# Kernel optimization log

Hardware: AMD Instinct MI355X
Metric: run time of the kernel (lower is better)

## Reference

```python
import jax, jax.numpy as jnp
import numpy as np

B, T, C, H = 4, 2048, 512, 8
D = C // H  # head dim = 64

def setup_inputs() -> dict:
    key = jax.random.key(0)
    ks = jax.random.split(key, 6)
    x = jax.random.normal(ks[0], (B, T, C), dtype=jnp.float32)
    # per-batch graph adjacency mask: True = attend, False = masked
    adj_matrix = jax.random.bernoulli(ks[1], 0.5, (B, T, T))
    # ensure self-edges so no row is fully masked
    adj_matrix = adj_matrix | jnp.eye(T, dtype=bool)[None]
    s = 0.02
    w_qkv = jax.random.normal(ks[2], (C, 3 * C), dtype=jnp.float32) * s
    b_qkv = jnp.zeros((3 * C,), dtype=jnp.float32)
    w_proj = jax.random.normal(ks[3], (C, C), dtype=jnp.float32) * s
    b_proj = jnp.zeros((C,), dtype=jnp.float32)
    return {"x": x, "adj_matrix": adj_matrix, "w_qkv": w_qkv, "b_qkv": b_qkv,
            "w_proj": w_proj, "b_proj": b_proj}

def reference(x, adj_matrix, w_qkv, b_qkv, w_proj, b_proj):
    Bx, Tx, Cx = x.shape
    qkv = x @ w_qkv + b_qkv                       # [B,T,3C]
    q, k, v = jnp.split(qkv, 3, axis=-1)
    def heads(t):
        return t.reshape(Bx, Tx, H, D).transpose(0, 2, 1, 3)  # [B,H,T,D]
    q, k, v = heads(q), heads(k), heads(v)
    scale = 1.0 / jnp.sqrt(jnp.asarray(D, dtype=x.dtype))
    scores = jnp.einsum('bhtd,bhsd->bhts', q, k) * scale      # [B,H,T,T]
    neg = jnp.finfo(scores.dtype).min
    scores = jnp.where(adj_matrix[:, None, :, :], scores, neg)
    attn = jax.nn.softmax(scores, axis=-1)
    y = jnp.einsum('bhts,bhsd->bhtd', attn, v)                # [B,H,T,D]
    y = y.transpose(0, 2, 1, 3).reshape(Bx, Tx, Cx)           # [B,T,C]
    return y @ w_proj + b_proj
```

## Files before the change

### kernel.cpp

```cpp
#include <hip/hip_runtime.h>
#include <stdint.h>

typedef __attribute__((ext_vector_type(8))) __bf16 bf16x8;
typedef __attribute__((ext_vector_type(4))) __bf16 bf16x4;
typedef __attribute__((ext_vector_type(2))) __bf16 bf16x2;
typedef __attribute__((ext_vector_type(4))) float f32x4;
typedef __attribute__((ext_vector_type(16))) float f32x16;
typedef __attribute__((ext_vector_type(4))) unsigned u32x4;
typedef __attribute__((ext_vector_type(2))) int i32x2;

__device__ __forceinline__ unsigned short f2bf(float f) {
  unsigned u = __float_as_uint(f);
  u += 0x7FFFu + ((u >> 16) & 1u);
  return (unsigned short)(u >> 16);
}

__device__ __forceinline__ float exp2fast(float x) {
#if __has_builtin(__builtin_amdgcn_exp2f)
  return __builtin_amdgcn_exp2f(x);
#else
  return __expf(x * 0.6931471805599453f);
#endif
}

__device__ __forceinline__ void pl32swap(unsigned &a, unsigned &b) {
#if __has_builtin(__builtin_amdgcn_permlane32_swap)
  i32x2 r = __builtin_amdgcn_permlane32_swap((int)a, (int)b, false, false);
  a = (unsigned)r[0]; b = (unsigned)r[1];
#else
  asm volatile("v_permlane32_swap_b32 %0, %1" : "+v"(a), "+v"(b));
#endif
}

__device__ __forceinline__ int swz8(int r) { return (r & 7) ^ ((r >> 3) & 3); }

__device__ __forceinline__ void gload16(const unsigned short* src, unsigned short* ldsdst) {
  __builtin_amdgcn_global_load_lds(
      (const __attribute__((address_space(1))) unsigned int*)src,
      (__attribute__((address_space(3))) unsigned int*)ldsdst, 16, 0, 0);
}

__device__ __forceinline__ void stage8(const unsigned short* gbase, long long strideElems,
                                       unsigned short* ldsTile, int rowBase) {
  const int lane = threadIdx.x & 63;
  const int r = rowBase + (lane >> 3);
  const int oct = (lane & 7) ^ swz8(r);
  gload16(gbase + (long long)r * strideElems + oct * 8, ldsTile + rowBase * 64);
}


__global__ __launch_bounds__(256) void prep(const float* __restrict__ x,
                                            unsigned short* __restrict__ xb,
                                            const float* __restrict__ wq,
                                            unsigned short* __restrict__ wqt,
                                            const float* __restrict__ wp,
                                            unsigned short* __restrict__ wpt,
                                            const int* __restrict__ adj,
                                            unsigned long long* __restrict__ mb) {
  int blk = blockIdx.x;
  if (blk < 16384) {
    int tid = blk * 256 + threadIdx.x;
    int4 v = ((const int4*)adj)[tid];
    unsigned n = (v.x != 0 ? 1u : 0u) | (v.y != 0 ? 2u : 0u) |
                 (v.z != 0 ? 4u : 0u) | (v.w != 0 ? 8u : 0u);
    unsigned long long part = (unsigned long long)n << ((threadIdx.x & 15) * 4);
    part |= __shfl_xor(part, 1);
    part |= __shfl_xor(part, 2);
    part |= __shfl_xor(part, 4);
    part |= __shfl_xor(part, 8);
    if ((threadIdx.x & 15) == 0) mb[tid >> 4] = part;
    return;
  }
  blk -= 16384;
  if (blk < 4096) {
    int i = (blk * 256 + threadIdx.x) * 4;
    float4 v = *(const float4*)(x + i);
    ushort4 o;
    o.x = f2bf(v.x); o.y = f2bf(v.y); o.z = f2bf(v.z); o.w = f2bf(v.w);
    *(ushort4*)(xb + i) = o;
    return;
  }
  blk -= 4096;
  const float* w; unsigned short* wt; int N; int bx, by;
  if (blk < 768) { w = wq; wt = wqt; N = 1536; bx = blk & 15; by = blk >> 4; }
  else { blk -= 768; w = wp; wt = wpt; N = 512; bx = blk & 15; by = blk >> 4; }
  __shared__ float tile[32][33];
  int k0 = bx * 32, n0 = by * 32;
  int tx = threadIdx.x & 31, ty = threadIdx.x >> 5;
#pragma unroll
  for (int i = 0; i < 4; i++)
    tile[ty + i * 8][tx] = w[(long long)(k0 + ty + i * 8) * N + n0 + tx];
  __syncthreads();
#pragma unroll
  for (int i = 0; i < 4; i++)
    wt[(long long)(n0 + ty + i * 8) * 512 + k0 + tx] = f2bf(tile[tx][ty + i * 8]);
}


__device__ __forceinline__ void gemm_core(const unsigned short* __restrict__ A,
                                          const unsigned short* __restrict__ Wt,
                                          unsigned short* Al, unsigned short* Bl,
                                          int m0, int n0, f32x4 acc[4][4]) {
  const int lane = threadIdx.x & 63;
  const int wid = threadIdx.x >> 6;
  const int c = lane & 15, g = lane >> 4;
  const int wm = wid >> 1, wn = wid & 1;
  const unsigned short* Ab = A + (long long)m0 * 512;
  const unsigned short* Bb = Wt + (long long)n0 * 512;

  for (int k0 = 0; k0 < 512; k0 += 64) {
    __syncthreads();
#pragma unroll
    for (int i = 0; i < 4; i++) stage8(Ab + k0, 512, Al, wid * 32 + i * 8);
#pragma unroll
    for (int i = 0; i < 4; i++) stage8(Bb + k0, 512, Bl, wid * 32 + i * 8);
    asm volatile("s_waitcnt vmcnt(0)" ::: "memory");
    __syncthreads();
#pragma unroll
    for (int kk = 0; kk < 2; kk++) {
      bf16x8 af[4], bfr[4];
#pragma unroll
      for (int mi = 0; mi < 4; mi++) {
        int row = wm * 64 + mi * 16 + c;
        af[mi] = *(const bf16x8*)&Al[row * 64 + (((kk << 2) | g) ^ swz8(row)) * 8];
      }
#pragma unroll
      for (int ni = 0; ni < 4; ni++) {
        int row = wn * 64 + ni * 16 + c;
        bfr[ni] = *(const bf16x8*)&Bl[row * 64 + (((kk << 2) | g) ^ swz8(row)) * 8];
      }
#pragma unroll
      for (int mi = 0; mi < 4; mi++)
#pragma unroll
        for (int ni = 0; ni < 4; ni++)
          acc[mi][ni] = __builtin_amdgcn_mfma_f32_16x16x32_bf16(af[mi], bfr[ni], acc[mi][ni], 0, 0, 0);
    }
  }
}

__global__ __launch_bounds__(256) void gemm_qkv(const unsigned short* __restrict__ xb,
                                                const unsigned short* __restrict__ wqt,
                                                const float* __restrict__ bqkv,
                                                unsigned short* __restrict__ qb,
                                                unsigned short* __restrict__ kb,
                                                unsigned short* __restrict__ vtb) {
  __shared__ __align__(16) unsigned short Al[128 * 64];
  __shared__ __align__(16) unsigned short Bl[128 * 64];
  f32x4 acc[4][4] = {};
  int m0 = blockIdx.x * 128, n0 = blockIdx.y * 128;
  gemm_core(xb, wqt, Al, Bl, m0, n0, acc);
  const int lane = threadIdx.x & 63;
  const int wid = threadIdx.x >> 6;
  const int c = lane & 15, g = lane >> 4;
  const int wm = wid >> 1, wn = wid & 1;
#pragma unroll
  for (int ni = 0; ni < 4; ni++) {
    int n = n0 + wn * 64 + ni * 16 + c;
    float bv = bqkv[n];
    int which = n >> 9;
    int h = (n & 511) >> 6, d = n & 63;
#pragma unroll
    for (int mi = 0; mi < 4; mi++) {
      int mbase = m0 + wm * 64 + mi * 16 + g * 4;
      int b = mbase >> 11, t0 = mbase & 2047;
      int bh = b * 8 + h;
      if (which == 2) {
        ushort4 o;
        o.x = f2bf(acc[mi][ni][0] + bv); o.y = f2bf(acc[mi][ni][1] + bv);
        o.z = f2bf(acc[mi][ni][2] + bv); o.w = f2bf(acc[mi][ni][3] + bv);
        *(ushort4*)&vtb[((long long)bh * 64 + d) * 2048 + t0] = o;
      } else if (which == 0) {
#pragma unroll
        for (int j = 0; j < 4; j++)
          qb[(bh * 2048 + t0 + j) * 64 + d] = f2bf((acc[mi][ni][j] + bv) * 0.18033688011112042f);
      } else {
#pragma unroll
        for (int j = 0; j < 4; j++)
          kb[(bh * 2048 + t0 + j) * 64 + d] = f2bf(acc[mi][ni][j] + bv);
      }
    }
  }
}

__global__ __launch_bounds__(256) void gemm_proj(const unsigned short* __restrict__ yb,
                                                 const unsigned short* __restrict__ wpt,
                                                 const float* __restrict__ bproj,
                                                 float* __restrict__ out) {
  __shared__ __align__(16) unsigned short Al[128 * 64];
  __shared__ __align__(16) unsigned short Bl[128 * 64];
  f32x4 acc[4][4] = {};
  int m0 = blockIdx.x * 128, n0 = blockIdx.y * 128;
  gemm_core(yb, wpt, Al, Bl, m0, n0, acc);
  const int lane = threadIdx.x & 63;
  const int wid = threadIdx.x >> 6;
  const int c = lane & 15, g = lane >> 4;
  const int wm = wid >> 1, wn = wid & 1;
#pragma unroll
  for (int ni = 0; ni < 4; ni++) {
    int n = n0 + wn * 64 + ni * 16 + c;
    float bv = bproj[n];
#pragma unroll
    for (int mi = 0; mi < 4; mi++) {
      int mbase = m0 + wm * 64 + mi * 16 + g * 4;
#pragma unroll
      for (int j = 0; j < 4; j++)
        out[(long long)(mbase + j) * 512 + n] = acc[mi][ni][j] + bv;
    }
  }
}

__global__ __launch_bounds__(256) void attn(const unsigned short* __restrict__ qb,
                                            const unsigned short* __restrict__ kb,
                                            const unsigned short* __restrict__ vtb,
                                            const unsigned long long* __restrict__ mbits,
                                            unsigned short* __restrict__ yb) {
  __shared__ __align__(16) unsigned short Kl[3][64 * 64];
  __shared__ __align__(16) unsigned short Vl[3][64 * 64];
  __shared__ __align__(16) float lut4[16][4];
  const int lane = threadIdx.x & 63;
  const int w = threadIdx.x >> 6;
  const int l31 = lane & 31, h5 = lane >> 5;
  const int sA = swz8(l31);
  const int bid = blockIdx.x;
  const int bh = bid & 31;
  const int q0 = (bid >> 5) * 128;
  const int b = bh >> 3, h = bh & 7;
  const int qglob = q0 + w * 32 + l31;

  if (threadIdx.x < 16) {
    int n = threadIdx.x;
#pragma unroll
    for (int j = 0; j < 4; j++) lut4[n][j] = ((n >> j) & 1) ? 0.0f : -1e30f;
  }
  __syncthreads();

  const unsigned short* qptr = qb + ((long long)bh * 2048 + qglob) * 64;
  bf16x8 qf[4];
#pragma unroll
  for (int cc = 0; cc < 4; cc++) qf[cc] = *(const bf16x8*)(qptr + cc * 16 + h5 * 8);

  const unsigned long long* mrow = mbits + ((long long)b * 2048 + qglob) * 32;

  const int ln8 = lane >> 3, o8 = lane & 7;
  const int rA = w * 16 + ln8, rB = rA + 8;
  const unsigned short* ksA = kb + (long long)bh * 2048 * 64 + rA * 64 + (o8 ^ swz8(rA)) * 8;
  const unsigned short* ksB = kb + (long long)bh * 2048 * 64 + rB * 64 + (o8 ^ swz8(rB)) * 8;
  const unsigned short* vsA = vtb + (long long)bh * 64 * 2048 + (long long)rA * 2048 + (o8 ^ swz8(rA)) * 8;
  const unsigned short* vsB = vtb + (long long)bh * 64 * 2048 + (long long)rB * 2048 + (o8 ^ swz8(rB)) * 8;
  const int ldA = w * 16 * 64, ldB = (w * 16 + 8) * 64;

  const int uo0 = ((0 + h5) ^ sA) * 8, uo1 = ((2 + h5) ^ sA) * 8;
  const int uo2 = ((4 + h5) ^ sA) * 8, uo3 = ((6 + h5) ^ sA) * 8;

  __bf16 onebf = (__bf16)1.0f;
  bf16x8 ones = {onebf, onebf, onebf, onebf, onebf, onebf, onebf, onebf};

  f32x16 accO0 = {0,0,0,0, 0,0,0,0, 0,0,0,0, 0,0,0,0};
  f32x16 accO1 = {0,0,0,0, 0,0,0,0, 0,0,0,0, 0,0,0,0};
  f32x16 lacc  = {0,0,0,0, 0,0,0,0, 0,0,0,0, 0,0,0,0};

#define STAGE_T(BI) do {                       \
    gload16(ksA, &Kl[BI][0] + ldA);            \
    gload16(ksB, &Kl[BI][0] + ldB);            \
    gload16(vsA, &Vl[BI][0] + ldA);            \
    gload16(vsB, &Vl[BI][0] + ldB);            \
    ksA += 4096; ksB += 4096; vsA += 64; vsB += 64; } while (0)

  auto COMPUTE = [&](const unsigned short* Kb, const unsigned short* Vb,
                     unsigned long long mwv) {
    unsigned lo = (unsigned)mwv, hi = (unsigned)(mwv >> 32);
    f32x16 st0, st1;
#pragma unroll
    for (int j = 0; j < 4; j++) {
      f32x4 s0 = *(const f32x4*)lut4[(lo >> (8 * j + 4 * h5)) & 0xF];
      f32x4 s1 = *(const f32x4*)lut4[(hi >> (8 * j + 4 * h5)) & 0xF];
#pragma unroll
      for (int i = 0; i < 4; i++) { st0[4 * j + i] = s0[i]; st1[4 * j + i] = s1[i]; }
    }
    __builtin_amdgcn_s_setprio(1);
#pragma unroll
    for (int cc = 0; cc < 4; cc++) {
      const int u = (cc == 0) ? uo0 : (cc == 1) ? uo1 : (cc == 2) ? uo2 : uo3;
      bf16x8 kf0 = *(const bf16x8*)&Kb[l31 * 64 + u];
      bf16x8 kf1 = *(const bf16x8*)&Kb[(32 + l31) * 64 + u];
      st0 = __builtin_amdgcn_mfma_f32_32x32x16_bf16(kf0, qf[cc], st0, 0, 0, 0);
      st1 = __builtin_amdgcn_mfma_f32_32x32x16_bf16(kf1, qf[cc], st1, 0, 0, 0);
    }
    __builtin_amdgcn_s_setprio(0);
    unsigned pd[2][8];
#pragma unroll
    for (int m = 0; m < 8; m++) {
      float p0 = exp2fast(st0[2 * m]);
      float p1 = exp2fast(st0[2 * m + 1]);
      float p2 = exp2fast(st1[2 * m]);
      float p3 = exp2fast(st1[2 * m + 1]);
      bf16x2 v0 = {(__bf16)p0, (__bf16)p1};
      bf16x2 v1 = {(__bf16)p2, (__bf16)p3};
      pd[0][m] = __builtin_bit_cast(unsigned, v0);
      pd[1][m] = __builtin_bit_cast(unsigned, v1);
    }
#pragma unroll
    for (int ot = 0; ot < 2; ot++)
#pragma unroll
      for (int hc = 0; hc < 2; hc++) {
        pl32swap(pd[ot][4 * hc + 0], pd[ot][4 * hc + 2]);
        pl32swap(pd[ot][4 * hc + 1], pd[ot][4 * hc + 3]);
      }
    __builtin_amdgcn_s_setprio(1);
#pragma unroll
    for (int cc = 0; cc < 4; cc++) {
      u32x4 pu = {pd[cc >> 1][4 * (cc & 1) + 0], pd[cc >> 1][4 * (cc & 1) + 1],
                  pd[cc >> 1][4 * (cc & 1) + 2], pd[cc >> 1][4 * (cc & 1) + 3]};
      bf16x8 pf = __builtin_bit_cast(bf16x8, pu);
      const int u = (cc == 0) ? uo0 : (cc == 1) ? uo1 : (cc == 2) ? uo2 : uo3;
      bf16x8 vf0 = *(const bf16x8*)&Vb[l31 * 64 + u];
      bf16x8 vf1 = *(const bf16x8*)&Vb[(32 + l31) * 64 + u];
      accO0 = __builtin_amdgcn_mfma_f32_32x32x16_bf16(vf0, pf, accO0, 0, 0, 0);
      accO1 = __builtin_amdgcn_mfma_f32_32x32x16_bf16(vf1, pf, accO1, 0, 0, 0);
      lacc  = __builtin_amdgcn_mfma_f32_32x32x16_bf16(ones, pf, lacc, 0, 0, 0);
    }
    __builtin_amdgcn_s_setprio(0);
  };

#define PHASE(TS, BS, BC, MSET, MUSE) do {                 \
    STAGE_T(BS);                                           \
    MSET = mrow[TS];                                       \
    __builtin_amdgcn_sched_barrier(0);                     \
    COMPUTE(&Kl[BC][0], &Vl[BC][0], MUSE);                 \
    asm volatile("s_waitcnt lgkmcnt(0)" ::: "memory");     \
    __builtin_amdgcn_sched_barrier(0);                     \
    asm volatile("s_waitcnt vmcnt(5)" ::: "memory");       \
    __builtin_amdgcn_s_barrier();                          \
    __builtin_amdgcn_sched_barrier(0); } while (0)

  unsigned long long m0, m1, m2;
  __builtin_amdgcn_sched_barrier(0);
  STAGE_T(0); m0 = mrow[0];
  __builtin_amdgcn_sched_barrier(0);
  STAGE_T(1); m1 = mrow[1];
  __builtin_amdgcn_sched_barrier(0);
  asm volatile("s_waitcnt vmcnt(5)" ::: "memory");
  __builtin_amdgcn_s_barrier();
  __builtin_amdgcn_sched_barrier(0);

  for (int k = 0; k < 10; ++k) {
    PHASE(3 * k + 2, 2, 0, m2, m0);
    PHASE(3 * k + 3, 0, 1, m0, m1);
    PHASE(3 * k + 4, 1, 2, m1, m2);
  }
  COMPUTE(&Kl[0][0], &Vl[0][0], m0);
  asm volatile("s_waitcnt lgkmcnt(0)" ::: "memory");
  asm volatile("s_waitcnt vmcnt(0)" ::: "memory");
  __builtin_amdgcn_s_barrier();
  __builtin_amdgcn_sched_barrier(0);
  COMPUTE(&Kl[1][0], &Vl[1][0], m1);

#undef PHASE
#undef STAGE_T

  float linv = 1.0f / lacc[0];
  unsigned short* yrow = yb + ((long long)(b * 2048 + qglob)) * 512 + h * 64;
#pragma unroll
  for (int m = 0; m < 4; m++) {
    int d0 = 8 * m + 4 * h5;
    bf16x4 o0 = {(__bf16)(accO0[4 * m + 0] * linv), (__bf16)(accO0[4 * m + 1] * linv),
                 (__bf16)(accO0[4 * m + 2] * linv), (__bf16)(accO0[4 * m + 3] * linv)};
    bf16x4 o1 = {(__bf16)(accO1[4 * m + 0] * linv), (__bf16)(accO1[4 * m + 1] * linv),
                 (__bf16)(accO1[4 * m + 2] * linv), (__bf16)(accO1[4 * m + 3] * linv)};
    *(bf16x4*)&yrow[d0] = o0;
    *(bf16x4*)&yrow[32 + d0] = o1;
  }
}


extern "C" void kernel_launch(void* const* d_in, const int* in_sizes, int n_in,
                              void* d_out, int out_size, void* d_ws, size_t ws_size,
                              hipStream_t stream) {
  const float* x      = (const float*)d_in[0];
  const int*   adj    = (const int*)d_in[1];
  const float* w_qkv  = (const float*)d_in[2];
  const float* b_qkv  = (const float*)d_in[3];
  const float* w_proj = (const float*)d_in[4];
  const float* b_proj = (const float*)d_in[5];
  float* out = (float*)d_out;

  char* ws = (char*)d_ws;
  unsigned short* xb  = (unsigned short*)(ws);
  unsigned short* qb  = (unsigned short*)(ws + 8388608);
  unsigned short* kbf = (unsigned short*)(ws + 16777216);
  unsigned short* vtb = (unsigned short*)(ws + 25165824);
  unsigned short* wqt = (unsigned short*)(ws + 33554432);
  unsigned short* wpt = (unsigned short*)(ws + 35127296);
  unsigned long long* mb = (unsigned long long*)(ws + 35651584);
  unsigned short* yb = xb;

  prep<<<dim3(21504), dim3(256), 0, stream>>>(x, xb, w_qkv, wqt, w_proj, wpt, adj, mb);
  gemm_qkv<<<dim3(64, 12), dim3(256), 0, stream>>>(xb, wqt, b_qkv, qb, kbf, vtb);
  attn<<<dim3(512), dim3(256), 0, stream>>>(qb, kbf, vtb, mb, yb);
  gemm_proj<<<dim3(64, 4), dim3(256), 0, stream>>>(yb, wpt, b_proj, out);
}
```

Before: 113.4 us.

## Split attention KV range across two wave groups per block and merge partials

Doubles the attention block to 512 threads, with two halves of four waves each processing half of the key/value sequence using their own double-buffered LDS tiles. Partial output accumulators and row sums from the second half are exchanged through shared memory and combined by the first half before normalisation and store. This raises per-block parallelism (more waves per CU with 512 blocks on 256 CUs) and shortens each wave's serial KV loop. In exchange it drops from triple to double buffering, waits on vmcnt(0) every tile, and adds a reduction step through LDS.

```diff
diff --git a/kernel.cpp b/kernel.cpp
--- a/kernel.cpp
+++ b/kernel.cpp
@@ -209,45 +209,53 @@
   }
 }
 
-__global__ __launch_bounds__(256) void attn(const unsigned short* __restrict__ qb,
-                                            const unsigned short* __restrict__ kb,
-                                            const unsigned short* __restrict__ vtb,
-                                            const unsigned long long* __restrict__ mbits,
-                                            unsigned short* __restrict__ yb) {
-  __shared__ __align__(16) unsigned short Kl[3][64 * 64];
-  __shared__ __align__(16) unsigned short Vl[3][64 * 64];
+__global__ __launch_bounds__(512, 4) void attn(const unsigned short* __restrict__ qb,
+                                               const unsigned short* __restrict__ kb,
+                                               const unsigned short* __restrict__ vtb,
+                                               const unsigned long long* __restrict__ mbits,
+                                               unsigned short* __restrict__ yb) {
+  __shared__ __align__(16) unsigned short Kl[2][2][64 * 64];
+  __shared__ __align__(16) unsigned short Vl[2][2][64 * 64];
   __shared__ __align__(16) float lut4[16][4];
   const int lane = threadIdx.x & 63;
   const int w = threadIdx.x >> 6;
+  const int half = w >> 2;
+  const int wq = w & 3;
   const int l31 = lane & 31, h5 = lane >> 5;
   const int sA = swz8(l31);
   const int bid = blockIdx.x;
   const int bh = bid & 31;
   const int q0 = (bid >> 5) * 128;
   const int b = bh >> 3, h = bh & 7;
-  const int qglob = q0 + w * 32 + l31;
+  const int qglob = q0 + wq * 32 + l31;
+  const int kvbase = half * 1024;
 
   if (threadIdx.x < 16) {
     int n = threadIdx.x;
 #pragma unroll
     for (int j = 0; j < 4; j++) lut4[n][j] = ((n >> j) & 1) ? 0.0f : -1e30f;
   }
-  __syncthreads();
 
   const unsigned short* qptr = qb + ((long long)bh * 2048 + qglob) * 64;
   bf16x8 qf[4];
 #pragma unroll
   for (int cc = 0; cc < 4; cc++) qf[cc] = *(const bf16x8*)(qptr + cc * 16 + h5 * 8);
 
-  const unsigned long long* mrow = mbits + ((long long)b * 2048 + qglob) * 32;
+  const unsigned long long* mrow =
+      mbits + ((long long)b * 2048 + qglob) * 32 + half * 16;
 
   const int ln8 = lane >> 3, o8 = lane & 7;
-  const int rA = w * 16 + ln8, rB = rA + 8;
-  const unsigned short* ksA = kb + (long long)bh * 2048 * 64 + rA * 64 + (o8 ^ swz8(rA)) * 8;
-  const unsigned short* ksB = kb + (long long)bh * 2048 * 64 + rB * 64 + (o8 ^ swz8(rB)) * 8;
-  const unsigned short* vsA = vtb + (long long)bh * 64 * 2048 + (long long)rA * 2048 + (o8 ^ swz8(rA)) * 8;
-  const unsigned short* vsB = vtb + (long long)bh * 64 * 2048 + (long long)rB * 2048 + (o8 ^ swz8(rB)) * 8;
-  const int ldA = w * 16 * 64, ldB = (w * 16 + 8) * 64;
+  const int rA = wq * 16 + ln8, rB = rA + 8;
+  const unsigned short* ksA = kb + (long long)bh * 2048 * 64 + (long long)(kvbase + rA) * 64 + (o8 ^ swz8(rA)) * 8;
+  const unsigned short* ksB = kb + (long long)bh * 2048 * 64 + (long long)(kvbase + rB) * 64 + (o8 ^ swz8(rB)) * 8;
+  const unsigned short* vsA = vtb + (long long)bh * 64 * 2048 + (long long)rA * 2048 + kvbase + (o8 ^ swz8(rA)) * 8;
+  const unsigned short* vsB = vtb + (long long)bh * 64 * 2048 + (long long)rB * 2048 + kvbase + (o8 ^ swz8(rB)) * 8;
+  const int ldA = wq * 16 * 64, ldB = (wq * 16 + 8) * 64;
+
+  unsigned short* K0 = &Kl[half][0][0];
+  unsigned short* K1 = &Kl[half][1][0];
+  unsigned short* V0 = &Vl[half][0][0];
+  unsigned short* V1 = &Vl[half][1][0];
 
   const int uo0 = ((0 + h5) ^ sA) * 8, uo1 = ((2 + h5) ^ sA) * 8;
   const int uo2 = ((4 + h5) ^ sA) * 8, uo3 = ((6 + h5) ^ sA) * 8;
@@ -259,11 +267,11 @@
   f32x16 accO1 = {0,0,0,0, 0,0,0,0, 0,0,0,0, 0,0,0,0};
   f32x16 lacc  = {0,0,0,0, 0,0,0,0, 0,0,0,0, 0,0,0,0};
 
-#define STAGE_T(BI) do {                       \
-    gload16(ksA, &Kl[BI][0] + ldA);            \
-    gload16(ksB, &Kl[BI][0] + ldB);            \
-    gload16(vsA, &Vl[BI][0] + ldA);            \
-    gload16(vsB, &Vl[BI][0] + ldB);            \
+#define STAGE_T(KB, VB) do {                   \
+    gload16(ksA, (KB) + ldA);                  \
+    gload16(ksB, (KB) + ldB);                  \
+    gload16(vsA, (VB) + ldA);                  \
+    gload16(vsB, (VB) + ldB);                  \
     ksA += 4096; ksB += 4096; vsA += 64; vsB += 64; } while (0)
 
   auto COMPUTE = [&](const unsigned short* Kb, const unsigned short* Vb,
@@ -322,53 +330,65 @@
     __builtin_amdgcn_s_setprio(0);
   };
 
-#define PHASE(TS, BS, BC, MSET, MUSE) do {                 \
-    STAGE_T(BS);                                           \
-    MSET = mrow[TS];                                       \
-    __builtin_amdgcn_sched_barrier(0);                     \
-    COMPUTE(&Kl[BC][0], &Vl[BC][0], MUSE);                 \
+#define TILE_SYNC do {                                     \
     asm volatile("s_waitcnt lgkmcnt(0)" ::: "memory");     \
-    __builtin_amdgcn_sched_barrier(0);                     \
-    asm volatile("s_waitcnt vmcnt(5)" ::: "memory");       \
-    __builtin_amdgcn_s_barrier();                          \
-    __builtin_amdgcn_sched_barrier(0); } while (0)
-
-  unsigned long long m0, m1, m2;
-  __builtin_amdgcn_sched_barrier(0);
-  STAGE_T(0); m0 = mrow[0];
-  __builtin_amdgcn_sched_barrier(0);
-  STAGE_T(1); m1 = mrow[1];
-  __builtin_amdgcn_sched_barrier(0);
-  asm volatile("s_waitcnt vmcnt(5)" ::: "memory");
-  __builtin_amdgcn_s_barrier();
-  __builtin_amdgcn_sched_barrier(0);
-
-  for (int k = 0; k < 10; ++k) {
-    PHASE(3 * k + 2, 2, 0, m2, m0);
-    PHASE(3 * k + 3, 0, 1, m0, m1);
-    PHASE(3 * k + 4, 1, 2, m1, m2);
-  }
-  COMPUTE(&Kl[0][0], &Vl[0][0], m0);
-  asm volatile("s_waitcnt lgkmcnt(0)" ::: "memory");
-  asm volatile("s_waitcnt vmcnt(0)" ::: "memory");
-  __builtin_amdgcn_s_barrier();
-  __builtin_amdgcn_sched_barrier(0);
-  COMPUTE(&Kl[1][0], &Vl[1][0], m1);
-
-#undef PHASE
+    asm volatile("s_waitcnt vmcnt(0)" ::: "memory");       \
+    __builtin_amdgcn_s_barrier(); } while (0)
+
+  unsigned long long mA, mB;
+  STAGE_T(K0, V0); mA = mrow[0];
+  TILE_SYNC;
+
+  for (int k = 0; k < 7; ++k) {
+    STAGE_T(K1, V1); mB = mrow[2 * k + 1];
+    COMPUTE(K0, V0, mA);
+    TILE_SYNC;
+    STAGE_T(K0, V0); mA = mrow[2 * k + 2];
+    COMPUTE(K1, V1, mB);
+    TILE_SYNC;
+  }
+  STAGE_T(K1, V1); mB = mrow[15];
+  COMPUTE(K0, V0, mA);
+  TILE_SYNC;
+  COMPUTE(K1, V1, mB);
+
+#undef TILE_SYNC
 #undef STAGE_T
 
-  float linv = 1.0f / lacc[0];
-  unsigned short* yrow = yb + ((long long)(b * 2048 + qglob)) * 512 + h * 64;
-#pragma unroll
-  for (int m = 0; m < 4; m++) {
-    int d0 = 8 * m + 4 * h5;
-    bf16x4 o0 = {(__bf16)(accO0[4 * m + 0] * linv), (__bf16)(accO0[4 * m + 1] * linv),
-                 (__bf16)(accO0[4 * m + 2] * linv), (__bf16)(accO0[4 * m + 3] * linv)};
-    bf16x4 o1 = {(__bf16)(accO1[4 * m + 0] * linv), (__bf16)(accO1[4 * m + 1] * linv),
-                 (__bf16)(accO1[4 * m + 2] * linv), (__bf16)(accO1[4 * m + 3] * linv)};
-    *(bf16x4*)&yrow[d0] = o0;
-    *(bf16x4*)&yrow[32 + d0] = o1;
+  __syncthreads();
+  float* xch = (float*)&Kl[0][0][0];
+  if (half == 1) {
+    float* dst = xch + (wq * 64 + lane) * 36;
+#pragma unroll
+    for (int m = 0; m < 4; m++) {
+      f32x4 a = {accO0[4 * m + 0], accO0[4 * m + 1], accO0[4 * m + 2], accO0[4 * m + 3]};
+      f32x4 c = {accO1[4 * m + 0], accO1[4 * m + 1], accO1[4 * m + 2], accO1[4 * m + 3]};
+      *(f32x4*)(dst + 4 * m) = a;
+      *(f32x4*)(dst + 16 + 4 * m) = c;
+    }
+    dst[32] = lacc[0];
+  }
+  __syncthreads();
+  if (half == 0) {
+    const float* src = xch + (wq * 64 + lane) * 36;
+    float linv = 1.0f / (lacc[0] + src[32]);
+    unsigned short* yrow = yb + ((long long)(b * 2048 + qglob)) * 512 + h * 64;
+#pragma unroll
+    for (int m = 0; m < 4; m++) {
+      f32x4 a = *(const f32x4*)(src + 4 * m);
+      f32x4 c = *(const f32x4*)(src + 16 + 4 * m);
+      int d0 = 8 * m + 4 * h5;
+      bf16x4 o0 = {(__bf16)((accO0[4 * m + 0] + a[0]) * linv),
+                   (__bf16)((accO0[4 * m + 1] + a[1]) * linv),
+                   (__bf16)((accO0[4 * m + 2] + a[2]) * linv),
+                   (__bf16)((accO0[4 * m + 3] + a[3]) * linv)};
+      bf16x4 o1 = {(__bf16)((accO1[4 * m + 0] + c[0]) * linv),
+                   (__bf16)((accO1[4 * m + 1] + c[1]) * linv),
+                   (__bf16)((accO1[4 * m + 2] + c[2]) * linv),
+                   (__bf16)((accO1[4 * m + 3] + c[3]) * linv)};
+      *(bf16x4*)&yrow[d0] = o0;
+      *(bf16x4*)&yrow[32 + d0] = o1;
+    }
   }
 }
 
@@ -396,6 +416,6 @@
 
   prep<<<dim3(21504), dim3(256), 0, stream>>>(x, xb, w_qkv, wqt, w_proj, wpt, adj, mb);
   gemm_qkv<<<dim3(64, 12), dim3(256), 0, stream>>>(xb, wqt, b_qkv, qb, kbf, vtb);
-  attn<<<dim3(512), dim3(256), 0, stream>>>(qb, kbf, vtb, mb, yb);
+  attn<<<dim3(512), dim3(512), 0, stream>>>(qb, kbf, vtb, mb, yb);
   gemm_proj<<<dim3(64, 4), dim3(256), 0, stream>>>(yb, wpt, b_proj, out);
 }
```

After: 145.2 us. 1.28x slower.
